# Kernel optimization log

Hardware: AMD Instinct MI355X
Metric: run time of the kernel (lower is better)

The kernel has to match this reference:

```python
import jax, jax.numpy as jnp
import numpy as np
import math

B, S, D, H = 2, 2048, 1024, 16
DH = D // H
NEG = -1e9


def gelu(x):
    return 0.5 * x * (1.0 + jnp.tanh(math.sqrt(2.0 / math.pi) * (x + 0.044715 * x ** 3)))


def layernorm(x, g, b, eps=1e-6):
    # faithful to module: uses std (unbiased, N-1) and adds eps to std, not var
    mean = jnp.mean(x, axis=-1, keepdims=True)
    var = jnp.sum((x - mean) ** 2, axis=-1, keepdims=True) / (x.shape[-1] - 1)
    std = jnp.sqrt(var)
    return g * (x - mean) / (std + eps) + b


def setup_inputs() -> dict:
    key = jax.random.key(0)
    ks = jax.random.split(key, 13)
    sd = 0.02
    return {
        "x": jax.random.normal(ks[0], (B, S, D), jnp.float32),
        "w_attn": jax.random.normal(ks[1], (D, 3 * D), jnp.float32) * sd,
        "b_attn": jnp.zeros((3 * D,), jnp.float32),
        "w_aproj": jax.random.normal(ks[2], (D, D), jnp.float32) * sd,
        "b_aproj": jnp.zeros((D,), jnp.float32),
        "g1": jnp.ones((D,), jnp.float32),
        "b1": jnp.zeros((D,), jnp.float32),
        "w_fc": jax.random.normal(ks[3], (D, 4 * D), jnp.float32) * sd,
        "b_fc": jnp.zeros((4 * D,), jnp.float32),
        "w_mproj": jax.random.normal(ks[4], (4 * D, D), jnp.float32) * sd,
        "b_mproj": jnp.zeros((D,), jnp.float32),
        "g2": jnp.ones((D,), jnp.float32),
        "b2": jnp.zeros((D,), jnp.float32),
    }


def reference(x, w_attn, b_attn, w_aproj, b_aproj, g1, b1, w_fc, b_fc, w_mproj, b_mproj, g2, b2):
    # --- attention ---
    qkv = x @ w_attn + b_attn                       # [B,S,3D]
    q, k, v = jnp.split(qkv, 3, axis=2)
    q = q.reshape(B, S, H, DH).transpose(0, 2, 1, 3)  # [B,H,S,DH]
    k = k.reshape(B, S, H, DH).transpose(0, 2, 1, 3)
    v = v.reshape(B, S, H, DH).transpose(0, 2, 1, 3)
    w = jnp.einsum('bhqd,bhkd->bhqk', q, k) / math.sqrt(DH)
    mask = jnp.tril(jnp.ones((S, S), jnp.float32))[None, None]
    w = w * mask + NEG * (1.0 - mask)
    w = jax.nn.softmax(w, axis=-1)
    a = jnp.einsum('bhqk,bhkd->bhqd', w, v)         # [B,H,S,DH]
    a = a.transpose(0, 2, 1, 3).reshape(B, S, D)
    a = a @ w_aproj + b_aproj
    # --- postLN + MLP ---
    n = layernorm(x + a, g1, b1)
    h = gelu(n @ w_fc + b_fc)
    m = h @ w_mproj + b_mproj
    return layernorm(n + m, g2, b2)
```

## Files before the change

### kernel.cpp

```cpp
#include <hip/hip_runtime.h>
#include <type_traits>


typedef unsigned short u16;
typedef short s16x8 __attribute__((ext_vector_type(8)));
typedef unsigned short u16x4 __attribute__((ext_vector_type(4)));
typedef float f32x4 __attribute__((ext_vector_type(4)));
typedef float f32x16 __attribute__((ext_vector_type(16)));

__device__ __forceinline__ u16 f2b(float f) {
    union { float f; unsigned u; } x{f};
    unsigned r = x.u + 0x7FFFu + ((x.u >> 16) & 1u);
    return (u16)(r >> 16);
}

__device__ __forceinline__ float b2f(u16 v) {
    union { unsigned u; float f; } x;
    x.u = ((unsigned)v) << 16;
    return x.f;
}

__device__ __forceinline__ f32x4 mfma16(s16x8 a, s16x8 b, f32x4 c) {
    return __builtin_amdgcn_mfma_f32_16x16x32_bf16(a, b, c, 0, 0, 0);
}

__device__ __forceinline__ f32x16 mfma32(s16x8 a, s16x8 b, f32x16 c) {
    return __builtin_amdgcn_mfma_f32_32x32x16_bf16(a, b, c, 0, 0, 0);
}

__device__ __forceinline__ int cvtpk(float a, float b) {
    int r;
    asm("v_cvt_pk_bf16_f32 %0, %1, %2" : "=v"(r) : "v"(a), "v"(b));
    return r;
}

__device__ __forceinline__ void gld_lds16(const u16* g, const u16* l) {
    __builtin_amdgcn_global_load_lds(
        (const __attribute__((address_space(1))) void*)g,
        (__attribute__((address_space(3))) void*)l, 16, 0, 0);
}

__device__ __forceinline__ void hard_barrier() {
    __builtin_amdgcn_sched_barrier(0);
    __builtin_amdgcn_s_barrier();
    __builtin_amdgcn_sched_barrier(0);
}

__global__ __launch_bounds__(256) void cvt_bf16(const float* __restrict__ in,
                                                u16* __restrict__ out, int n4) {
    int i = blockIdx.x * 256 + threadIdx.x;
    if (i < n4) {
        float4 v = ((const float4*)in)[i];
        u16x4 o = {f2b(v.x), f2b(v.y), f2b(v.z), f2b(v.w)};
        ((u16x4*)out)[i] = o;
    }
}

__global__ __launch_bounds__(256) void transpose_bf16(const float* __restrict__ W,
                                                      u16* __restrict__ WT,
                                                      int K, int N) {
    __shared__ float t[32][33];
    int tx = threadIdx.x & 31, ty = threadIdx.x >> 5;
    int n0 = blockIdx.x * 32, k0 = blockIdx.y * 32;
    #pragma unroll
    for (int r = ty; r < 32; r += 8)
        t[r][tx] = W[(size_t)(k0 + r) * N + n0 + tx];
    __syncthreads();
    #pragma unroll
    for (int r = ty; r < 32; r += 8)
        WT[(size_t)(n0 + r) * K + k0 + tx] = f2b(t[tx][r]);
}

__global__ __launch_bounds__(256) void tr_v(const u16* __restrict__ qkv,
                                            u16* __restrict__ vT) {
    __shared__ u16 tile[64 * 64];
    int t = threadIdx.x;
    int bh = blockIdx.x & 31, st = blockIdx.x >> 5;
    int b = bh >> 4, h = bh & 15;
    int s0 = st * 64;
    int r = t >> 2, c4 = (t & 3) * 16;
    const u16* src = qkv + (size_t)b * 2048 * 3072 + (size_t)(s0 + r) * 3072
                   + 2048 + h * 64 + c4;
    s16x8 a0 = *(const s16x8*)src;
    s16x8 a1 = *(const s16x8*)(src + 8);
    int xr = (r & 7) << 3;
    *(s16x8*)&tile[r * 64 + (c4 ^ xr)] = a0;
    *(s16x8*)&tile[r * 64 + ((c4 + 8) ^ xr)] = a1;
    __syncthreads();
    int d = t >> 2, s4 = (t & 3) * 16;
    u16 buf[16];
    #pragma unroll
    for (int j = 0; j < 16; ++j) {
        int s = s4 + j;
        buf[j] = tile[s * 64 + (d ^ ((s & 7) << 3))];
    }
    u16* dst = vT + (size_t)(bh * 64 + d) * 2048 + s0 + s4;
    *(s16x8*)dst = *(s16x8*)&buf[0];
    *(s16x8*)(dst + 8) = *(s16x8*)&buf[8];
}

template<int BN, bool GELU, typename OT>
__global__ __launch_bounds__(512) void gemm_pl(const u16* __restrict__ A,
                                               const u16* __restrict__ BT,
                                               const float* __restrict__ bias,
                                               OT* __restrict__ C,
                                               int M, int N, int K, int ldc) {
    constexpr int NF = BN / 64;
    constexpr int BNI = BN / 64;
    constexpr int LTOT = 2 + BNI;
    __shared__ u16 As[2][128 * 64];
    __shared__ u16 Bs[2][BN * 64];

    int t = threadIdx.x;
    int w = t >> 6, l = t & 63, l16 = l & 15, lh = l >> 4;
    int wr = w >> 2, wc = w & 3;

    int nbm = M >> 7;
    int cpx = gridDim.x >> 3;
    int id = blockIdx.x;
    int id2 = (id & 7) * cpx + (id >> 3);
    size_t m0 = (size_t)(id2 % nbm) * 128;
    size_t n0 = (size_t)(id2 / nbm) * BN;

    int rowA = t >> 3;
    int gc2 = (t & 7) ^ (rowA & 7);
    const u16* Ag = A + (m0 + rowA) * (size_t)K + gc2 * 8;
    const u16* Bg = BT + (n0 + rowA) * (size_t)K + gc2 * 8;
    int wb = w * 512;

    f32x4 acc[4][NF] = {};
    int rx = (l16 & 7) * 8;

    #pragma unroll
    for (int j = 0; j < 2; ++j)
        gld_lds16(Ag + (size_t)j * 64 * K, &As[0][j * 4096 + wb]);
    #pragma unroll
    for (int j = 0; j < BNI; ++j)
        gld_lds16(Bg + (size_t)j * 64 * K, &Bs[0][j * 4096 + wb]);
    #pragma unroll
    for (int j = 0; j < 2; ++j)
        gld_lds16(Ag + 64 + (size_t)j * 64 * K, &As[1][j * 4096 + wb]);
    #pragma unroll
    for (int j = 0; j < BNI; ++j)
        gld_lds16(Bg + 64 + (size_t)j * 64 * K, &Bs[1][j * 4096 + wb]);

#define GTILE(CB, kk, LAST)                                                   \
    {                                                                         \
        if (LAST) asm volatile("s_waitcnt vmcnt(0)" ::: "memory");            \
        else      asm volatile("s_waitcnt vmcnt(%0)" :: "n"(LTOT) : "memory");\
        hard_barrier();                                                       \
        __builtin_amdgcn_s_setprio(1);                                        \
        _Pragma("unroll")                                                     \
        for (int ks = 0; ks < 2; ++ks) {                                      \
            s16x8 af[4], bf[NF];                                              \
            _Pragma("unroll")                                                 \
            for (int fm = 0; fm < 4; ++fm) {                                  \
                int row = wr * 64 + fm * 16 + l16;                            \
                int col = ((ks * 4 + lh) * 8) ^ rx;                           \
                af[fm] = *(const s16x8*)&As[CB][row * 64 + col];              \
            }                                                                 \
            _Pragma("unroll")                                                 \
            for (int fn = 0; fn < NF; ++fn) {                                 \
                int row = wc * (BN / 4) + fn * 16 + l16;                      \
                int col = ((ks * 4 + lh) * 8) ^ rx;                           \
                bf[fn] = *(const s16x8*)&Bs[CB][row * 64 + col];              \
            }                                                                 \
            _Pragma("unroll")                                                 \
            for (int fm = 0; fm < 4; ++fm)                                    \
                _Pragma("unroll")                                             \
                for (int fn = 0; fn < NF; ++fn)                               \
                    acc[fm][fn] = mfma16(af[fm], bf[fn], acc[fm][fn]);        \
        }                                                                     \
        __builtin_amdgcn_s_setprio(0);                                        \
        hard_barrier();                                                       \
        if ((kk) + 128 < K) {                                                 \
            const u16* Ap = Ag + (kk) + 128;                                  \
            _Pragma("unroll")                                                 \
            for (int j = 0; j < 2; ++j)                                       \
                gld_lds16(Ap + (size_t)j * 64 * K, &As[CB][j * 4096 + wb]);   \
            const u16* Bp = Bg + (kk) + 128;                                  \
            _Pragma("unroll")                                                 \
            for (int j = 0; j < BNI; ++j)                                     \
                gld_lds16(Bp + (size_t)j * 64 * K, &Bs[CB][j * 4096 + wb]);   \
        }                                                                     \
    }

    for (int k0 = 0; k0 < K; k0 += 128) {
        GTILE(0, k0, (k0 + 64 >= K))
        GTILE(1, k0 + 64, (k0 + 128 >= K))
    }
#undef GTILE

    #pragma unroll
    for (int fn = 0; fn < NF; ++fn) {
        size_t col = n0 + wc * (BN / 4) + fn * 16 + l16;
        float bs = bias[col];
        #pragma unroll
        for (int fm = 0; fm < 4; ++fm) {
            size_t row0 = m0 + wr * 64 + fm * 16 + lh * 4;
            #pragma unroll
            for (int i = 0; i < 4; ++i) {
                float v = acc[fm][fn][i] + bs;
                if constexpr (GELU) {
                    float x3 = v * v * v;
                    v = 0.5f * v * (1.f + tanhf(0.7978845608f * (v + 0.044715f * x3)));
                }
                if constexpr (std::is_same<OT, u16>::value)
                    C[(row0 + i) * ldc + col] = f2b(v);
                else
                    C[(row0 + i) * ldc + col] = v;
            }
        }
    }
}

__global__ __launch_bounds__(256) void attn_kernel(const u16* __restrict__ qkv,
                                                   const u16* __restrict__ vT,
                                                   u16* __restrict__ p0,
                                                   u16* __restrict__ p1,
                                                   u16* __restrict__ p2,
                                                   u16* __restrict__ p3,
                                                   float2* __restrict__ stats) {
    constexpr int S = 2048, D3 = 3072, Dm = 1024;
    __shared__ u16 Kl[2][64 * 64];
    __shared__ u16 Vt[2][64 * 64];

    int t = threadIdx.x;
    int w = t >> 6, l = t & 63;
    int l32 = l & 31, hi = l >> 5;
    int bid = blockIdx.x;
    int bh = bid & 31;
    int pr = (bid >> 5) & 7;
    int quar = bid >> 8;
    int b = bh >> 4, h = bh & 15;
    size_t base = (size_t)b * S * D3;

    u16* pout = quar == 0 ? p0 : (quar == 1 ? p1 : (quar == 2 ? p2 : p3));

    int rK0 = t >> 3, gK = t & 7;
    int rK1 = rK0 + 32;
    size_t koff0 = (size_t)rK0 * D3 + (size_t)((gK ^ (rK0 & 7)) * 8);
    size_t koff1 = (size_t)rK1 * D3 + (size_t)((gK ^ (rK1 & 7)) * 8);
    const u16* kbase = qkv + base + Dm + h * 64;
    size_t voff0 = (size_t)(bh * 64 + rK0) * 2048 + (size_t)((gK ^ (rK0 & 7)) * 8);
    size_t voff1 = (size_t)(bh * 64 + 32 + rK0) * 2048 + (size_t)((gK ^ (rK0 & 7)) * 8);

    constexpr float cexp = 0.18033688011112042f;
    constexpr float THR = 64.0f;
    int xg = l32 & 7;

#define STAGE(SC, BUF)                                                        \
    {                                                                         \
        size_t ko_ = (size_t)(SC) * 64 * D3;                                  \
        int kvb_ = (SC) * 64;                                                 \
        gld_lds16(kbase + ko_ + koff0, &Kl[BUF][w * 512]);                    \
        gld_lds16(kbase + ko_ + koff1, &Kl[BUF][2048 + w * 512]);             \
        gld_lds16(vT + voff0 + kvb_, &Vt[BUF][w * 512]);                      \
        gld_lds16(vT + voff1 + kvb_, &Vt[BUF][2048 + w * 512]);               \
    }

    #pragma unroll 1
    for (int ph = 0; ph < 2; ++ph) {
        int qt = ph ? (15 - pr) : pr;
        int qb = qt * 128 + w * 32;
        int nst = 2 * (qt + 1);
        int c0 = (nst * quar) >> 2;
        int c1 = (nst * (quar + 1)) >> 2;

        f32x16 O0 = {}, O1 = {};
        float m = -1e30f, lr = 0.f;

        if (c0 < c1) {
            s16x8 qf[4];
            const u16* qp = qkv + base + (size_t)(qb + l32) * D3 + h * 64 + hi * 8;
            #pragma unroll
            for (int kk = 0; kk < 4; ++kk)
                qf[kk] = *(const s16x8*)(qp + kk * 16);

            STAGE(c0, 0)
            if (c0 + 1 < c1) STAGE(c0 + 1, 1)

            int cur = 0;
            #pragma unroll 1
            for (int sc = c0; sc < c1; ++sc) {
                if (sc + 1 < c1)
                    asm volatile("s_waitcnt vmcnt(4)" ::: "memory");
                else
                    asm volatile("s_waitcnt vmcnt(0)" ::: "memory");
                hard_barrier();

                int kvb = sc * 64;
                int navail = ((qb - kvb) >> 5) + 1;
                if (navail > 0) {
                    if (navail > 2) navail = 2;
                    const u16* Kc = Kl[cur];
                    const u16* Vc = Vt[cur];
                    f32x16 sa0 = {}, sa1 = {};
                    #pragma unroll
                    for (int kk = 0; kk < 4; ++kk) {
                        s16x8 kf = *(const s16x8*)&Kc[l32 * 64 + (((2 * kk + hi) ^ xg) * 8)];
                        sa0 = mfma32(kf, qf[kk], sa0);
                    }
                    if (navail == 2) {
                        #pragma unroll
                        for (int kk = 0; kk < 4; ++kk) {
                            s16x8 kf = *(const s16x8*)&Kc[(32 + l32) * 64 + (((2 * kk + hi) ^ xg) * 8)];
                            sa1 = mfma32(kf, qf[kk], sa1);
                        }
                    }
                    bool diag0 = (kvb == qb);
                    bool diag1 = (kvb + 32 == qb);
                    float p[32];
                    float mx = -1e30f;
                    #pragma unroll
                    for (int reg = 0; reg < 16; ++reg) {
                        int kvloc = (reg & 3) + 8 * (reg >> 2) + 4 * hi;
                        float s0 = sa0[reg];
                        if (diag0 && kvloc > l32) s0 = -1e30f;
                        p[reg] = s0;
                        mx = fmaxf(mx, s0);
                    }
                    if (navail == 2) {
                        #pragma unroll
                        for (int reg = 0; reg < 16; ++reg) {
                            int kvloc = (reg & 3) + 8 * (reg >> 2) + 4 * hi;
                            float s1 = sa1[reg];
                            if (diag1 && kvloc > l32) s1 = -1e30f;
                            p[16 + reg] = s1;
                            mx = fmaxf(mx, s1);
                        }
                    }
                    mx = fmaxf(mx, __shfl_xor(mx, 32));
                    if (!__all(mx <= m + THR)) {
                        float mn = fmaxf(m, mx);
                        float a_ = exp2f(cexp * (m - mn));
                        m = mn;
                        #pragma unroll
                        for (int reg = 0; reg < 16; ++reg) {
                            int src = (reg & 3) + 8 * (reg >> 2) + 4 * hi;
                            float aq = __shfl(a_, src);
                            O0[reg] *= aq;
                            O1[reg] *= aq;
                        }
                        lr *= a_;
                    }
                    float cm = cexp * m;
                    float rs = 0.f;
                    #pragma unroll
                    for (int reg = 0; reg < 16; ++reg) {
                        p[reg] = exp2f(fmaf(cexp, p[reg], -cm));
                        rs += p[reg];
                    }
                    if (navail == 2) {
                        #pragma unroll
                        for (int reg = 16; reg < 32; ++reg) {
                            p[reg] = exp2f(fmaf(cexp, p[reg], -cm));
                            rs += p[reg];
                        }
                    }
                    rs += __shfl_xor(rs, 32);
                    lr += rs;

                    #pragma unroll
                    for (int c = 0; c < 4; ++c) {
                        if (c < navail * 2) {
                            int pb = (c >> 1) * 16 + (c & 1) * 8;
                            int pk01 = cvtpk(p[pb + 0], p[pb + 1]);
                            int pk23 = cvtpk(p[pb + 2], p[pb + 3]);
                            int pk45 = cvtpk(p[pb + 4], p[pb + 5]);
                            int pk67 = cvtpk(p[pb + 6], p[pb + 7]);
                            int sx01 = __shfl_xor(pk01, 32);
                            int sx23 = __shfl_xor(pk23, 32);
                            int sx45 = __shfl_xor(pk45, 32);
                            int sx67 = __shfl_xor(pk67, 32);
                            union { int i[4]; s16x8 v; } u;
                            u.i[0] = hi ? sx45 : pk01;
                            u.i[1] = hi ? sx67 : pk23;
                            u.i[2] = hi ? pk45 : sx01;
                            u.i[3] = hi ? pk67 : sx23;
                            int go = ((c * 2 + hi) ^ xg) * 8;
                            s16x8 vb0 = *(const s16x8*)&Vc[l32 * 64 + go];
                            O0 = mfma32(u.v, vb0, O0);
                            s16x8 vb1 = *(const s16x8*)&Vc[(32 + l32) * 64 + go];
                            O1 = mfma32(u.v, vb1, O1);
                        }
                    }
                }

                hard_barrier();
                if (sc + 2 < c1) STAGE(sc + 2, cur)
                cur ^= 1;
            }
        }

        size_t obase = (size_t)b * S * 1024 + h * 64;
        #pragma unroll
        for (int reg = 0; reg < 16; ++reg) {
            int src = (reg & 3) + 8 * (reg >> 2) + 4 * hi;
            size_t row = obase + (size_t)(qb + src) * 1024;
            pout[row + l32] = f2b(O0[reg]);
            pout[row + 32 + l32] = f2b(O1[reg]);
        }
        if (hi == 0) {
            float2 st; st.x = m; st.y = lr;
            stats[quar * 65536 + ((b * 2048 + qb + l32) * 16 + h)] = st;
        }
    }
#undef STAGE
}

__global__ __launch_bounds__(256) void merge_attn(u16* __restrict__ p0,
                                                  const u16* __restrict__ p1,
                                                  const u16* __restrict__ p2,
                                                  const u16* __restrict__ p3,
                                                  const float2* __restrict__ stats) {
    constexpr float cexp = 0.18033688011112042f;
    int gid = blockIdx.x * 256 + threadIdx.x;
    int rh = gid >> 2;
    int dc = (gid & 3) * 16;
    int R = rh >> 4, h = rh & 15;
    size_t addr = (size_t)R * 1024 + h * 64 + dc;

    float2 s0 = stats[rh];
    float2 s1 = stats[65536 + rh];
    float2 s2 = stats[131072 + rh];
    float2 s3 = stats[196608 + rh];
    float M = fmaxf(fmaxf(s0.x, s1.x), fmaxf(s2.x, s3.x));
    float a0 = exp2f(cexp * (s0.x - M));
    float a1 = exp2f(cexp * (s1.x - M));
    float a2 = exp2f(cexp * (s2.x - M));
    float a3 = exp2f(cexp * (s3.x - M));
    float inv = 1.f / (a0 * s0.y + a1 * s1.y + a2 * s2.y + a3 * s3.y);
    a0 *= inv; a1 *= inv; a2 *= inv; a3 *= inv;

    u16x4 o[4];
    #pragma unroll
    for (int j = 0; j < 4; ++j) {
        u16x4 q0 = *(const u16x4*)(p0 + addr + j * 4);
        u16x4 q1 = *(const u16x4*)(p1 + addr + j * 4);
        u16x4 q2 = *(const u16x4*)(p2 + addr + j * 4);
        u16x4 q3 = *(const u16x4*)(p3 + addr + j * 4);
        #pragma unroll
        for (int e = 0; e < 4; ++e)
            o[j][e] = f2b(a0 * b2f(q0[e]) + a1 * b2f(q1[e]) +
                          a2 * b2f(q2[e]) + a3 * b2f(q3[e]));
    }
    #pragma unroll
    for (int j = 0; j < 4; ++j)
        *(u16x4*)(p0 + addr + j * 4) = o[j];
}

template<bool WB>
__global__ __launch_bounds__(256) void resln(const float* __restrict__ xa,
                                             const float* __restrict__ xb2,
                                             const float* __restrict__ g,
                                             const float* __restrict__ be,
                                             float* __restrict__ outf,
                                             u16* __restrict__ outb) {
    int row = blockIdx.x;
    int t = threadIdx.x;
    size_t base = (size_t)row * 1024 + t * 4;
    float4 va = *(const float4*)(xa + base);
    float4 vb = *(const float4*)(xb2 + base);
    float v0 = va.x + vb.x, v1 = va.y + vb.y, v2 = va.z + vb.z, v3 = va.w + vb.w;
    float s1 = v0 + v1 + v2 + v3;
    float s2 = v0 * v0 + v1 * v1 + v2 * v2 + v3 * v3;
    #pragma unroll
    for (int off = 32; off >= 1; off >>= 1) {
        s1 += __shfl_down(s1, off);
        s2 += __shfl_down(s2, off);
    }
    __shared__ float r1[4], r2[4];
    if ((t & 63) == 0) { r1[t >> 6] = s1; r2[t >> 6] = s2; }
    __syncthreads();
    s1 = r1[0] + r1[1] + r1[2] + r1[3];
    s2 = r2[0] + r2[1] + r2[2] + r2[3];
    float mean = s1 * (1.f / 1024.f);
    float var = fmaxf((s2 - 1024.f * mean * mean) * (1.f / 1023.f), 0.f);
    float inv = 1.f / (sqrtf(var) + 1e-6f);
    int col = t * 4;
    float y0 = g[col + 0] * ((v0 - mean) * inv) + be[col + 0];
    float y1 = g[col + 1] * ((v1 - mean) * inv) + be[col + 1];
    float y2 = g[col + 2] * ((v2 - mean) * inv) + be[col + 2];
    float y3 = g[col + 3] * ((v3 - mean) * inv) + be[col + 3];
    float4 o = {y0, y1, y2, y3};
    *(float4*)(outf + base) = o;
    if constexpr (WB) {
        u16x4 ob = {f2b(y0), f2b(y1), f2b(y2), f2b(y3)};
        *(u16x4*)(outb + base) = ob;
    }
}

extern "C" void kernel_launch(void* const* d_in, const int* in_sizes, int n_in,
                              void* d_out, int out_size, void* d_ws, size_t ws_size,
                              hipStream_t stream) {
    (void)in_sizes; (void)n_in; (void)out_size; (void)ws_size;
    const float* x       = (const float*)d_in[0];
    const float* w_attn  = (const float*)d_in[1];
    const float* b_attn  = (const float*)d_in[2];
    const float* w_aproj = (const float*)d_in[3];
    const float* b_aproj = (const float*)d_in[4];
    const float* g1      = (const float*)d_in[5];
    const float* b1      = (const float*)d_in[6];
    const float* w_fc    = (const float*)d_in[7];
    const float* b_fc    = (const float*)d_in[8];
    const float* w_mproj = (const float*)d_in[9];
    const float* b_mproj = (const float*)d_in[10];
    const float* g2      = (const float*)d_in[11];
    const float* b2      = (const float*)d_in[12];
    float* out = (float*)d_out;

    constexpr int M = 4096;
    constexpr int D = 1024;

    char* ws = (char*)d_ws;
    u16*   slotA = (u16*)ws;
    char*  pB    = ws + (32u << 20);
    char*  pC    = ws + (40u << 20);
    char*  pD    = ws + (48u << 20);
    char*  pE    = ws + (64u << 20);

    u16*   xb    = (u16*)pB;
    u16*   wT    = (u16*)pC;
    u16*   qkv   = slotA;
    u16*   vT    = slotA + (24u << 20) / 2;
    u16*   part0 = (u16*)pB;
    u16*   part1 = (u16*)pC;
    u16*   part2 = (u16*)pD;
    u16*   part3 = (u16*)(pD + (8u << 20));
    float2* stat = (float2*)pE;
    u16*   abuf  = (u16*)pB;
    float* aout  = (float*)pD;
    float* nbuf  = (float*)pE;
    u16*   nb    = (u16*)pB;
    u16*   h     = slotA;
    float* mout  = (float*)pD;

    dim3 blk(256);
    dim3 blk512(512);

    cvt_bf16<<<dim3(4096), blk, 0, stream>>>(x, xb, M * D / 4);

    transpose_bf16<<<dim3(3072 / 32, 1024 / 32), blk, 0, stream>>>(w_attn, wT, 1024, 3072);
    gemm_pl<128, false, u16><<<dim3((M / 128) * (3072 / 128)), blk512, 0, stream>>>(
        xb, wT, b_attn, qkv, M, 3072, 1024, 3072);

    tr_v<<<dim3(1024), blk, 0, stream>>>(qkv, vT);
    attn_kernel<<<dim3(1024), blk, 0, stream>>>(qkv, vT, part0, part1, part2, part3, stat);
    merge_attn<<<dim3(1024), blk, 0, stream>>>(part0, part1, part2, part3, stat);

    transpose_bf16<<<dim3(1024 / 32, 1024 / 32), blk, 0, stream>>>(w_aproj, wT, 1024, 1024);
    gemm_pl<64, false, float><<<dim3((M / 128) * (1024 / 64)), blk512, 0, stream>>>(
        abuf, wT, b_aproj, aout, M, 1024, 1024, 1024);

    resln<true><<<dim3(M), blk, 0, stream>>>(x, aout, g1, b1, nbuf, nb);

    transpose_bf16<<<dim3(4096 / 32, 1024 / 32), blk, 0, stream>>>(w_fc, wT, 1024, 4096);
    gemm_pl<128, true, u16><<<dim3((M / 128) * (4096 / 128)), blk512, 0, stream>>>(
        nb, wT, b_fc, h, M, 4096, 1024, 4096);

    transpose_bf16<<<dim3(1024 / 32, 4096 / 32), blk, 0, stream>>>(w_mproj, wT, 4096, 1024);
    gemm_pl<64, false, float><<<dim3((M / 128) * (1024 / 64)), blk512, 0, stream>>>(
        h, wT, b_mproj, mout, M, 1024, 4096, 1024);

    resln<false><<<dim3(M), blk, 0, stream>>>(nbuf, mout, g2, b2, out, nullptr);
}
```

Before: 271.7 us.

## Fuse V transpose into QKV GEMM epilogue, remap attention blocks, skip mask off-diagonal

The QKV GEMM epilogue now also writes the V columns transposed into vT, packing four consecutive rows per store, so the separate tr_v kernel and its extra pass over V are gone. The attention kernel's block-index decode is reordered so that neighbouring blocks cover different heads and quarters. The causal-mask check is also hoisted into a single branch so that off-diagonal tiles take a mask-free path. The fused epilogue adds strided 8-byte global stores in the QKV GEMM.

```diff
diff --git a/kernel.cpp b/kernel.cpp
--- a/kernel.cpp
+++ b/kernel.cpp
@@ -71,39 +71,12 @@
         WT[(size_t)(n0 + r) * K + k0 + tx] = f2b(t[tx][r]);
 }
 
-__global__ __launch_bounds__(256) void tr_v(const u16* __restrict__ qkv,
-                                            u16* __restrict__ vT) {
-    __shared__ u16 tile[64 * 64];
-    int t = threadIdx.x;
-    int bh = blockIdx.x & 31, st = blockIdx.x >> 5;
-    int b = bh >> 4, h = bh & 15;
-    int s0 = st * 64;
-    int r = t >> 2, c4 = (t & 3) * 16;
-    const u16* src = qkv + (size_t)b * 2048 * 3072 + (size_t)(s0 + r) * 3072
-                   + 2048 + h * 64 + c4;
-    s16x8 a0 = *(const s16x8*)src;
-    s16x8 a1 = *(const s16x8*)(src + 8);
-    int xr = (r & 7) << 3;
-    *(s16x8*)&tile[r * 64 + (c4 ^ xr)] = a0;
-    *(s16x8*)&tile[r * 64 + ((c4 + 8) ^ xr)] = a1;
-    __syncthreads();
-    int d = t >> 2, s4 = (t & 3) * 16;
-    u16 buf[16];
-    #pragma unroll
-    for (int j = 0; j < 16; ++j) {
-        int s = s4 + j;
-        buf[j] = tile[s * 64 + (d ^ ((s & 7) << 3))];
-    }
-    u16* dst = vT + (size_t)(bh * 64 + d) * 2048 + s0 + s4;
-    *(s16x8*)dst = *(s16x8*)&buf[0];
-    *(s16x8*)(dst + 8) = *(s16x8*)&buf[8];
-}
-
-template<int BN, bool GELU, typename OT>
+template<int BN, bool GELU, typename OT, bool VW = false>
 __global__ __launch_bounds__(512) void gemm_pl(const u16* __restrict__ A,
                                                const u16* __restrict__ BT,
                                                const float* __restrict__ bias,
                                                OT* __restrict__ C,
+                                               u16* __restrict__ vTout,
                                                int M, int N, int K, int ldc) {
     constexpr int NF = BN / 64;
     constexpr int BNI = BN / 64;
@@ -198,6 +171,7 @@
         #pragma unroll
         for (int fm = 0; fm < 4; ++fm) {
             size_t row0 = m0 + wr * 64 + fm * 16 + lh * 4;
+            u16x4 pack;
             #pragma unroll
             for (int i = 0; i < 4; ++i) {
                 float v = acc[fm][fn][i] + bs;
@@ -205,10 +179,21 @@
                     float x3 = v * v * v;
                     v = 0.5f * v * (1.f + tanhf(0.7978845608f * (v + 0.044715f * x3)));
                 }
-                if constexpr (std::is_same<OT, u16>::value)
-                    C[(row0 + i) * ldc + col] = f2b(v);
-                else
+                if constexpr (std::is_same<OT, u16>::value) {
+                    u16 q = f2b(v);
+                    C[(row0 + i) * ldc + col] = q;
+                    pack[i] = q;
+                } else {
                     C[(row0 + i) * ldc + col] = v;
+                }
+            }
+            if constexpr (VW) {
+                if (n0 >= 2048) {
+                    int hh = ((int)col - 2048) >> 6;
+                    int dd = ((int)col - 2048) & 63;
+                    size_t vrow = (size_t)(((row0 >> 11) * 16 + hh) * 64 + dd);
+                    *(u16x4*)(vTout + vrow * 2048 + (row0 & 2047)) = pack;
+                }
             }
         }
     }
@@ -229,9 +214,10 @@
     int w = t >> 6, l = t & 63;
     int l32 = l & 31, hi = l >> 5;
     int bid = blockIdx.x;
-    int bh = bid & 31;
-    int pr = (bid >> 5) & 7;
-    int quar = bid >> 8;
+    int bh = (bid & 7) * 4 + ((bid >> 3) & 3);
+    int rest = bid >> 5;
+    int quar = rest & 3;
+    int pr = rest >> 2;
     int b = bh >> 4, h = bh & 15;
     size_t base = (size_t)b * S * D3;
 
@@ -312,22 +298,37 @@
                     bool diag1 = (kvb + 32 == qb);
                     float p[32];
                     float mx = -1e30f;
-                    #pragma unroll
-                    for (int reg = 0; reg < 16; ++reg) {
-                        int kvloc = (reg & 3) + 8 * (reg >> 2) + 4 * hi;
-                        float s0 = sa0[reg];
-                        if (diag0 && kvloc > l32) s0 = -1e30f;
-                        p[reg] = s0;
-                        mx = fmaxf(mx, s0);
-                    }
-                    if (navail == 2) {
+                    if (diag0 | diag1) {
                         #pragma unroll
                         for (int reg = 0; reg < 16; ++reg) {
                             int kvloc = (reg & 3) + 8 * (reg >> 2) + 4 * hi;
-                            float s1 = sa1[reg];
-                            if (diag1 && kvloc > l32) s1 = -1e30f;
-                            p[16 + reg] = s1;
-                            mx = fmaxf(mx, s1);
+                            float s0 = sa0[reg];
+                            if (diag0 && kvloc > l32) s0 = -1e30f;
+                            p[reg] = s0;
+                            mx = fmaxf(mx, s0);
+                        }
+                        if (navail == 2) {
+                            #pragma unroll
+                            for (int reg = 0; reg < 16; ++reg) {
+                                int kvloc = (reg & 3) + 8 * (reg >> 2) + 4 * hi;
+                                float s1 = sa1[reg];
+                                if (diag1 && kvloc > l32) s1 = -1e30f;
+                                p[16 + reg] = s1;
+                                mx = fmaxf(mx, s1);
+                            }
+                        }
+                    } else {
+                        #pragma unroll
+                        for (int reg = 0; reg < 16; ++reg) {
+                            p[reg] = sa0[reg];
+                            mx = fmaxf(mx, sa0[reg]);
+                        }
+                        if (navail == 2) {
+                            #pragma unroll
+                            for (int reg = 0; reg < 16; ++reg) {
+                                p[16 + reg] = sa1[reg];
+                                mx = fmaxf(mx, sa1[reg]);
+                            }
                         }
                     }
                     mx = fmaxf(mx, __shfl_xor(mx, 32));
@@ -542,26 +543,25 @@
     cvt_bf16<<<dim3(4096), blk, 0, stream>>>(x, xb, M * D / 4);
 
     transpose_bf16<<<dim3(3072 / 32, 1024 / 32), blk, 0, stream>>>(w_attn, wT, 1024, 3072);
-    gemm_pl<128, false, u16><<<dim3((M / 128) * (3072 / 128)), blk512, 0, stream>>>(
-        xb, wT, b_attn, qkv, M, 3072, 1024, 3072);
-
-    tr_v<<<dim3(1024), blk, 0, stream>>>(qkv, vT);
+    gemm_pl<128, false, u16, true><<<dim3((M / 128) * (3072 / 128)), blk512, 0, stream>>>(
+        xb, wT, b_attn, qkv, vT, M, 3072, 1024, 3072);
+
     attn_kernel<<<dim3(1024), blk, 0, stream>>>(qkv, vT, part0, part1, part2, part3, stat);
     merge_attn<<<dim3(1024), blk, 0, stream>>>(part0, part1, part2, part3, stat);
 
     transpose_bf16<<<dim3(1024 / 32, 1024 / 32), blk, 0, stream>>>(w_aproj, wT, 1024, 1024);
     gemm_pl<64, false, float><<<dim3((M / 128) * (1024 / 64)), blk512, 0, stream>>>(
-        abuf, wT, b_aproj, aout, M, 1024, 1024, 1024);
+        abuf, wT, b_aproj, aout, nullptr, M, 1024, 1024, 1024);
 
     resln<true><<<dim3(M), blk, 0, stream>>>(x, aout, g1, b1, nbuf, nb);
 
     transpose_bf16<<<dim3(4096 / 32, 1024 / 32), blk, 0, stream>>>(w_fc, wT, 1024, 4096);
     gemm_pl<128, true, u16><<<dim3((M / 128) * (4096 / 128)), blk512, 0, stream>>>(
-        nb, wT, b_fc, h, M, 4096, 1024, 4096);
+        nb, wT, b_fc, h, nullptr, M, 4096, 1024, 4096);
 
     transpose_bf16<<<dim3(1024 / 32, 4096 / 32), blk, 0, stream>>>(w_mproj, wT, 4096, 1024);
     gemm_pl<64, false, float><<<dim3((M / 128) * (1024 / 64)), blk512, 0, stream>>>(
-        h, wT, b_mproj, mout, M, 1024, 4096, 1024);
+        h, wT, b_mproj, mout, nullptr, M, 1024, 4096, 1024);
 
     resln<false><<<dim3(M), blk, 0, stream>>>(nbuf, mout, g2, b2, out, nullptr);
 }
```

New measurement: 272.3 us. About the same (+0.2%).
